# Optimization experiments

Measured on AMD Instinct MI355X. Metric: run time of the kernel, lower is better.

Reference implementation:

```python
import jax, jax.numpy as jnp
import numpy as np
import math

NUM_BINS = 10
TAIL_BOUND = 5.0
FILTER_CHANNELS = 192
KERNEL_SIZE = 3
N_LAYERS = 3
HALF = 1
MIN_BIN = 1e-3
MIN_DERIV = 1e-3


def conv1d(x, w, b, dilation=1, groups=1, padding=0):
    # x: [B,C,T], w: [O, C//groups, K]
    y = jax.lax.conv_general_dilated(
        x, w, window_strides=(1,), padding=[(padding, padding)],
        rhs_dilation=(dilation,), dimension_numbers=('NCH', 'OIH', 'NCH'),
        feature_group_count=groups)
    return y + b[None, :, None]


def ln_channels(x, g, b, eps=1e-5):
    # LayerNorm over channel dim (VITS modules.LayerNorm)
    m = jnp.mean(x, axis=1, keepdims=True)
    v = jnp.mean((x - m) ** 2, axis=1, keepdims=True)
    return g[None, :, None] * (x - m) * jax.lax.rsqrt(v + eps) + b[None, :, None]


def rq_spline(x1, uw, uh, ud):
    # piecewise rational-quadratic transform with linear tails (Durkan et al.)
    # x1: [B,1,T]; uw,uh: [B,1,T,K]; ud: [B,1,T,K-1]
    K = NUM_BINS
    tb = TAIL_BOUND
    inside = (x1 >= -tb) & (x1 <= tb)

    const = math.log(math.exp(1.0 - MIN_DERIV) - 1.0)  # softplus^-1(1-min_d)
    ud = jnp.pad(ud, [(0, 0)] * (ud.ndim - 1) + [(1, 1)], constant_values=const)

    widths = jax.nn.softmax(uw, axis=-1)
    widths = MIN_BIN + (1.0 - MIN_BIN * K) * widths
    cumw = jnp.pad(jnp.cumsum(widths, -1), [(0, 0)] * (uw.ndim - 1) + [(1, 0)])
    cumw = 2.0 * tb * cumw - tb
    cumw = cumw.at[..., 0].set(-tb).at[..., -1].set(tb)
    widths = cumw[..., 1:] - cumw[..., :-1]

    heights = jax.nn.softmax(uh, axis=-1)
    heights = MIN_BIN + (1.0 - MIN_BIN * K) * heights
    cumh = jnp.pad(jnp.cumsum(heights, -1), [(0, 0)] * (uh.ndim - 1) + [(1, 0)])
    cumh = 2.0 * tb * cumh - tb
    cumh = cumh.at[..., 0].set(-tb).at[..., -1].set(tb)
    heights = cumh[..., 1:] - cumh[..., :-1]

    derivs = MIN_DERIV + jax.nn.softplus(ud)  # [..., K+1]

    xin = jnp.clip(x1, -tb, tb)  # clamp so out-of-range lanes stay finite
    locs = cumw.at[..., -1].add(1e-6)
    bin_idx = jnp.clip(jnp.sum((xin[..., None] >= locs).astype(jnp.int32), -1) - 1, 0, K - 1)

    def take(a):
        return jnp.take_along_axis(a, bin_idx[..., None], axis=-1)[..., 0]

    icw = take(cumw)
    iw = take(widths)
    ich = take(cumh)
    ih = take(heights)
    d_l = take(derivs[..., :-1])
    d_r = take(derivs[..., 1:])
    delta = ih / iw

    theta = (xin - icw) / iw
    t1m = theta * (1.0 - theta)
    numerator = ih * (delta * theta * theta + d_l * t1m)
    denominator = delta + (d_l + d_r - 2.0 * delta) * t1m
    y = ich + numerator / denominator
    dnum = (delta * delta) * (d_r * theta * theta + 2.0 * delta * t1m + d_l * (1.0 - theta) ** 2)
    lad = jnp.log(dnum) - 2.0 * jnp.log(denominator)

    out = jnp.where(inside, y, x1)       # linear tails: identity outside
    lad = jnp.where(inside, lad, 0.0)
    return out, lad


def reference(x, x_mask, pre_w, pre_b, sep_w, sep_b, pw_w, pw_b,
              ln1_g, ln1_b, ln2_g, ln2_b, proj_w, proj_b):
    x0, x1 = x[:, :HALF], x[:, HALF:]
    h = conv1d(x0, pre_w, pre_b)
    # DDSConv (dilated depth-separable conv stack), p_dropout=0
    for i in range(N_LAYERS):
        d = KERNEL_SIZE ** i
        pad = (KERNEL_SIZE * d - d) // 2
        y = conv1d(h * x_mask, sep_w[i], sep_b[i], dilation=d,
                   groups=FILTER_CHANNELS, padding=pad)
        y = jax.nn.gelu(ln_channels(y, ln1_g[i], ln1_b[i]), approximate=False)
        y = conv1d(y, pw_w[i], pw_b[i])
        y = jax.nn.gelu(ln_channels(y, ln2_g[i], ln2_b[i]), approximate=False)
        h = h + y
    h = h * x_mask
    h = conv1d(h, proj_w, proj_b) * x_mask  # [B, half*(3K-1), T]
    b, c, t = x0.shape
    h = h.reshape(b, c, -1, t).transpose(0, 1, 3, 2)  # [B, half, T, 3K-1]
    scale = math.sqrt(FILTER_CHANNELS)
    uw = h[..., :NUM_BINS] / scale
    uh = h[..., NUM_BINS:2 * NUM_BINS] / scale
    ud = h[..., 2 * NUM_BINS:]
    x1o, lad = rq_spline(x1, uw, uh, ud)
    out = jnp.concatenate([x0, x1o], axis=1) * x_mask
    logdet = jnp.sum(lad * x_mask, axis=(1, 2))
    return out, logdet


def setup_inputs() -> dict:
    key = jax.random.key(0)
    ks = jax.random.split(key, 8)
    B, T, C, L, K = 64, 4096, FILTER_CHANNELS, N_LAYERS, KERNEL_SIZE
    return {
        'x': jax.random.normal(ks[0], (B, 2, T), jnp.float32),
        'x_mask': jnp.ones((B, 1, T), jnp.float32),
        'pre_w': jax.random.normal(ks[1], (C, 1, 1), jnp.float32) * 0.1,
        'pre_b': jnp.zeros((C,), jnp.float32),
        'sep_w': jax.random.normal(ks[2], (L, C, 1, K), jnp.float32) * 0.1,
        'sep_b': jnp.zeros((L, C), jnp.float32),
        'pw_w': jax.random.normal(ks[3], (L, C, C, 1), jnp.float32) * (1.0 / np.sqrt(C).astype(np.float32)),
        'pw_b': jnp.zeros((L, C), jnp.float32),
        'ln1_g': jnp.ones((L, C), jnp.float32),
        'ln1_b': jnp.zeros((L, C), jnp.float32),
        'ln2_g': jnp.ones((L, C), jnp.float32),
        'ln2_b': jnp.zeros((L, C), jnp.float32),
        'proj_w': jax.random.normal(ks[4], (HALF * (3 * NUM_BINS - 1), C, 1), jnp.float32) * 0.01,
        'proj_b': jnp.zeros((HALF * (3 * NUM_BINS - 1),), jnp.float32),
    }
```

## Files before the change

### kernel.cpp

```cpp
#include <hip/hip_runtime.h>
#include <stdint.h>

#define TT_ 4096
#define CC_ 192
#define TILE_ 64
#define HALO_ 13
#define TW_ 90
#define HS_ 100
#define YTS_ 200
#define NT_ 512

typedef float f32x4 __attribute__((ext_vector_type(4)));
typedef short s16x4 __attribute__((ext_vector_type(4)));
typedef short s16x8 __attribute__((ext_vector_type(8)));
typedef uint32_t ui32x2 __attribute__((ext_vector_type(2)));
typedef uint32_t ui32x4 __attribute__((ext_vector_type(4)));

__device__ __forceinline__ float bf2f(short s){
  uint32_t u = ((uint32_t)(uint16_t)s) << 16;
  float f; __builtin_memcpy(&f, &u, 4); return f;
}
__device__ __forceinline__ float bfhalf(uint32_t u, int hi){
  uint32_t v = hi ? (u & 0xFFFF0000u) : (u << 16);
  float f; __builtin_memcpy(&f, &v, 4); return f;
}
__device__ __forceinline__ short f2bf(float f){
  uint32_t u; __builtin_memcpy(&u, &f, 4);
  u += 0x7FFFu + ((u >> 16) & 1u);
  return (short)(u >> 16);
}
__device__ __forceinline__ uint32_t fbits(float f){
  uint32_t u; __builtin_memcpy(&u, &f, 4); return u;
}
__device__ __forceinline__ uint32_t pk_trunc(float lo, float hi){
  return __builtin_amdgcn_perm(fbits(hi), fbits(lo), 0x07060302u);
}
__device__ __forceinline__ uint32_t rne_u(float f){
  uint32_t u = fbits(f);
  return u + 0x7FFFu + ((u >> 16) & 1u);
}
__device__ __forceinline__ uint32_t pk_rne(float lo, float hi){
  return __builtin_amdgcn_perm(rne_u(hi), rne_u(lo), 0x07060302u);
}
__device__ __forceinline__ float gelu_f(float x){
  float t = x*x;
  float p = x*__builtin_fmaf(t, 0.0713548162f, 1.5957691216f);
  float e = __expf(-p);
  return x * __builtin_amdgcn_rcpf(1.0f + e);
}
__device__ __forceinline__ int ytix(int row, int col){
  return row*YTS_ + ((((col >> 3) ^ (row & 3)) << 3) | (col & 7));
}

template<int D>
__device__ __forceinline__ void dw_pass(const short* __restrict__ Hs, short* __restrict__ YTs,
    const float* __restrict__ sw, const float* __restrict__ sb,
    int jlo, int jhi, int tid){
  constexpr int WO = (D==9) ? 16 : 8;
  constexpr int NU = (D==9) ? 20 : 12;
  for (int g = tid; g < 96*12; g += NT_){
    int cg = g % 96, jg = g / 96;
    int j0 = jg*8;
    if (j0 + 8 <= jlo || j0 >= jhi) continue;
    int c0 = cg*2;
    uint32_t wpa[NU], wpb[NU];
    {
      const uint32_t* ra = (const uint32_t*)(Hs + (c0+0)*HS_ + j0 - WO);
      const uint32_t* rb = (const uint32_t*)(Hs + (c0+1)*HS_ + j0 - WO);
      #pragma unroll
      for (int u = 0; u < NU/2; ++u){
        ui32x2 ta = *(const ui32x2*)(ra + u*2);
        ui32x2 tb = *(const ui32x2*)(rb + u*2);
        wpa[u*2] = ta[0]; wpa[u*2+1] = ta[1];
        wpb[u*2] = tb[0]; wpb[u*2+1] = tb[1];
      }
    }
    float w0a = sw[c0*3+0], w1a = sw[c0*3+1], w2a = sw[c0*3+2], bav = sb[c0];
    float w0b = sw[c0*3+3], w1b = sw[c0*3+4], w2b = sw[c0*3+5], bbv = sb[c0+1];
    #pragma unroll
    for (int j = 0; j < 8; ++j){
      int h0 = WO + j - D, h1 = WO + j, h2 = WO + j + D;
      float va = __builtin_fmaf(w0a, bfhalf(wpa[h0>>1], h0&1),
                 __builtin_fmaf(w1a, bfhalf(wpa[h1>>1], h1&1),
                 __builtin_fmaf(w2a, bfhalf(wpa[h2>>1], h2&1), bav)));
      float vb = __builtin_fmaf(w0b, bfhalf(wpb[h0>>1], h0&1),
                 __builtin_fmaf(w1b, bfhalf(wpb[h1>>1], h1&1),
                 __builtin_fmaf(w2b, bfhalf(wpb[h2>>1], h2&1), bbv)));
      *(uint32_t*)(YTs + ytix(j0+j, c0)) = pk_trunc(va, vb);
    }
  }
}

__device__ __forceinline__ void ln_stats(const short* __restrict__ YTs, float* __restrict__ SM,
                                         float* __restrict__ SR, int jlo, int jhi, int tid){
  if (tid < 384){
    int row = tid >> 2, qtr = tid & 3;
    if (row >= jlo && row < jhi){
      float s0 = 0.f, s1 = 0.f, q0 = 0.f, q1 = 0.f;
      #pragma unroll
      for (int u=0;u<6;++u){
        s16x8 v = *(const s16x8*)(YTs + ytix(row, qtr*48 + u*8));
        #pragma unroll
        for (int e=0;e<4;e++){ float f=bf2f(v[e]); s0 += f; q0 = __builtin_fmaf(f,f,q0); }
        #pragma unroll
        for (int e=4;e<8;e++){ float f=bf2f(v[e]); s1 += f; q1 = __builtin_fmaf(f,f,q1); }
      }
      float s = s0+s1, q = q0+q1;
      s += __shfl_xor(s,1); q += __shfl_xor(q,1);
      s += __shfl_xor(s,2); q += __shfl_xor(q,2);
      if (qtr==0){
        float mean = s*(1.f/192.f);
        float var = fmaxf(q*(1.f/192.f) - mean*mean, 0.f);
        SM[row]=mean; SR[row]=rsqrtf(var+1e-5f);
      }
    }
  }
}

__global__ __launch_bounds__(512, 4)
void convflow_main(
    const float* __restrict__ x, const float* __restrict__ xmask,
    const float* __restrict__ pre_w, const float* __restrict__ pre_b,
    const float* __restrict__ sep_w, const float* __restrict__ sep_b,
    const float* __restrict__ pw_b,
    const float* __restrict__ ln1_g, const float* __restrict__ ln1_b,
    const float* __restrict__ ln2_g, const float* __restrict__ ln2_b,
    const float* __restrict__ proj_b,
    const short* __restrict__ Wbf, const short* __restrict__ Pbf,
    float* __restrict__ out, float* __restrict__ part)
{
  __shared__ __align__(16) char smem_raw[78592];
  float* MB = (float*)(smem_raw + 0);
  float* XB = (float*)(smem_raw + 640);
  float* SM = (float*)(smem_raw + 1024);
  float* SR = (float*)(smem_raw + 1408);
  short* H  = (short*)(smem_raw + 1792);
  short* YT = (short*)(smem_raw + 40192);
  float* HP = (float*)(smem_raw + 65792);

  const int tid = threadIdx.x;
  const int b = blockIdx.y, tile = blockIdx.x;
  const int t0 = tile*TILE_ - HALO_;

  for (int idx = tid; idx < 160; idx += NT_){
    int j = idx - 16; int t = t0 + j;
    float m = 0.f;
    if (j >= 0 && j < TW_ && t >= 0 && t < TT_) m = xmask[b*TT_ + t];
    MB[idx] = m;
  }
  if (tid < 96){
    int t = t0 + tid; float v = 0.f;
    if (tid < TW_ && t >= 0 && t < TT_) v = x[(b*2)*TT_ + t];
    XB[tid] = v;
  }
  __syncthreads();

  for (int g = tid; g < CC_*24; g += NT_){
    int jq = g % 24, c = g / 24;
    float w = pre_w[c], bb = pre_b[c];
    int j0 = jq*4;
    float v0 = (w*XB[j0+0] + bb)*MB[16+j0+0];
    float v1 = (w*XB[j0+1] + bb)*MB[16+j0+1];
    float v2 = (w*XB[j0+2] + bb)*MB[16+j0+2];
    float v3 = (w*XB[j0+3] + bb)*MB[16+j0+3];
    ui32x2 o; o[0] = pk_rne(v0, v1); o[1] = pk_rne(v2, v3);
    *(ui32x2*)(H + c*HS_ + j0) = o;
  }
  __syncthreads();

  #pragma unroll 1
  for (int li = 0; li < 3; ++li){
    const int jlo = (li==0) ? 1 : ((li==1) ? 4 : 13);
    const int jhi = (li==0) ? 89 : ((li==1) ? 86 : 77);
    const float* sw = sep_w + li*CC_*3;
    const float* sb = sep_b + li*CC_;

    if (li == 0)      dw_pass<1>(H, YT, sw, sb, jlo, jhi, tid);
    else if (li == 1) dw_pass<3>(H, YT, sw, sb, jlo, jhi, tid);
    else              dw_pass<9>(H, YT, sw, sb, jlo, jhi, tid);
    __syncthreads();

    ln_stats(YT, SM, SR, jlo, jhi, tid); __syncthreads();

    {
      const float* g1 = ln1_g + li*CC_;
      const float* b1 = ln1_b + li*CC_;
      for (int g = tid; g < 96*24; g += NT_){
        int ch = g % 24, row = g / 24;
        short* p = YT + ytix(row, ch*8);
        if (row >= jlo && row < jhi){
          float m = SM[row], r = SR[row];
          s16x8 v = *(s16x8*)p;
          f32x4 ga = *(const f32x4*)&g1[ch*8], gb = *(const f32x4*)&g1[ch*8+4];
          f32x4 ba = *(const f32x4*)&b1[ch*8], bb = *(const f32x4*)&b1[ch*8+4];
          float ov[8];
          #pragma unroll
          for (int e=0;e<4;e++){
            float val = (bf2f(v[e]) - m)*r*ga[e] + ba[e];
            ov[e] = gelu_f(val);
          }
          #pragma unroll
          for (int e=4;e<8;e++){
            float val = (bf2f(v[e]) - m)*r*gb[e-4] + bb[e-4];
            ov[e] = gelu_f(val);
          }
          ui32x4 o;
          #pragma unroll
          for (int e=0;e<4;e++) o[e] = pk_trunc(ov[2*e], ov[2*e+1]);
          *(ui32x4*)p = o;
        } else {
          ui32x4 z = {0u,0u,0u,0u};
          *(ui32x4*)p = z;
        }
      }
    }
    __syncthreads();

    {
      int w = tid >> 6, lane = tid & 63, l16 = lane & 15, q = lane >> 4;
      int Mh = w & 3, Nh = w >> 2;
      f32x4 acc[3][3];
      #pragma unroll
      for (int r=0;r<3;r++)
        #pragma unroll
        for (int s=0;s<3;s++){ f32x4 z = {0.f,0.f,0.f,0.f}; acc[r][s] = z; }
      const short* Wl = Wbf + li*CC_*CC_;
      #pragma unroll
      for (int kk=0;kk<6;++kk){
        s16x8 bv[3], av[3];
        #pragma unroll
        for (int s=0;s<3;++s)
          bv[s] = *(const s16x8*)&YT[ytix((Nh*3+s)*16 + l16, kk*32 + q*8)];
        #pragma unroll
        for (int r=0;r<3;++r)
          av[r] = *(const s16x8*)&Wl[((Mh*3+r)*16 + l16)*CC_ + kk*32 + q*8];
        #pragma unroll
        for (int r=0;r<3;++r)
          #pragma unroll
          for (int s=0;s<3;++s)
            acc[r][s] = __builtin_amdgcn_mfma_f32_16x16x32_bf16(av[r], bv[s], acc[r][s], 0, 0, 0);
      }
      __syncthreads();
      #pragma unroll
      for (int r=0;r<3;++r){
        int m0 = (Mh*3+r)*16 + q*4;
        f32x4 bias = *(const f32x4*)&pw_b[li*CC_ + m0];
        #pragma unroll
        for (int s=0;s<3;++s){
          int n = (Nh*3+s)*16 + l16;
          ui32x2 ov;
          ov[0] = pk_trunc(acc[r][s][0]+bias[0], acc[r][s][1]+bias[1]);
          ov[1] = pk_trunc(acc[r][s][2]+bias[2], acc[r][s][3]+bias[3]);
          *(ui32x2*)(YT + ytix(n, m0)) = ov;
        }
      }
      __syncthreads();
    }

    ln_stats(YT, SM, SR, jlo, jhi, tid); __syncthreads();

    {
      const float* g2 = ln2_g + li*CC_;
      const float* b2 = ln2_b + li*CC_;
      for (int g = tid; g < 24*48; g += NT_){
        int cgp = g % 48, jg = g / 48;
        int j0 = jg*4, c0 = cgp*4;
        if (j0 + 4 <= jlo || j0 >= jhi) continue;
        f32x4 mv = *(f32x4*)&SM[j0], rv = *(f32x4*)&SR[j0];
        f32x4 mk = *(f32x4*)&MB[16 + j0];
        f32x4 gv = *(const f32x4*)&g2[c0], bv = *(const f32x4*)&b2[c0];
        s16x4 yr[4];
        #pragma unroll
        for (int jj=0;jj<4;++jj) yr[jj] = *(s16x4*)(YT + ytix(j0+jj, c0));
        #pragma unroll
        for (int cc=0;cc<4;++cc){
          short* hp_ = H + (c0+cc)*HS_ + j0;
          s16x4 hv = *(s16x4*)hp_;
          float hf[4];
          #pragma unroll
          for (int jj=0;jj<4;++jj){
            int j = j0 + jj;
            float val = (bf2f(yr[jj][cc]) - mv[jj])*rv[jj]*gv[cc] + bv[cc];
            float hn = (bf2f(hv[jj]) + gelu_f(val))*mk[jj];
            bool ok = (j >= jlo) && (j < jhi);
            hf[jj] = ok ? hn : bf2f(hv[jj]);
          }
          ui32x2 o; o[0] = pk_rne(hf[0], hf[1]); o[1] = pk_rne(hf[2], hf[3]);
          *(ui32x2*)hp_ = o;
        }
      }
    }
    __syncthreads();
  }

  {
    int w = tid >> 6;
    if (w < 4){
      int lane = tid & 63, l16 = lane & 15, q = lane >> 4;
      int mt = w >> 1, ntp = w & 1;
      f32x4 pacc[2];
      { f32x4 z = {0.f,0.f,0.f,0.f}; pacc[0] = z; pacc[1] = z; }
      #pragma unroll
      for (int kk=0;kk<6;++kk){
        s16x8 a = *(const s16x8*)&Pbf[(mt*16 + l16)*CC_ + kk*32 + q*8];
        #pragma unroll
        for (int s=0;s<2;++s){
          int n = (ntp*2+s)*16 + l16;
          s16x8 bvv;
          #pragma unroll
          for (int i=0;i<8;++i)
            bvv[i] = H[(kk*32 + q*8 + i)*HS_ + HALO_ + n];
          pacc[s] = __builtin_amdgcn_mfma_f32_16x16x32_bf16(a, bvv, pacc[s], 0, 0, 0);
        }
      }
      #pragma unroll
      for (int s=0;s<2;++s)
        #pragma unroll
        for (int e=0;e<4;e++){
          int m = mt*16 + q*4 + e;
          if (m < 29){
            int n = (ntp*2+s)*16 + l16;
            HP[n*33 + m] = (pacc[s][e] + proj_b[m]) * MB[16 + HALO_ + n];
          }
        }
    }
  }
  __syncthreads();

  if (tid < 64){
    const int n = tid;
    const int tg = tile*TILE_ + n;
    const float msk = MB[16 + HALO_ + n];
    const float* hp = &HP[n*33];
    const float inv_s = 0.07216878364870323f;
    float uw[10], uh[10], ud9[9];
    #pragma unroll
    for (int k=0;k<10;k++){ uw[k] = hp[k]*inv_s; uh[k] = hp[10+k]*inv_s; }
    #pragma unroll
    for (int k=0;k<9;k++) ud9[k] = hp[20+k];

    float cumw[11], cumh[11];
    {
      float mx = uw[0];
      #pragma unroll
      for (int k=1;k<10;k++) mx = fmaxf(mx, uw[k]);
      float ex[10]; float ss = 0.f;
      #pragma unroll
      for (int k=0;k<10;k++){ ex[k] = __expf(uw[k]-mx); ss += ex[k]; }
      float inv = 1.0f/ss;
      cumw[0] = -5.f; float cw = 0.f;
      #pragma unroll
      for (int k=0;k<10;k++){ float wk = 0.001f + 0.99f*(ex[k]*inv); cw += wk; cumw[k+1] = 10.f*cw - 5.f; }
      cumw[10] = 5.f;
    }
    {
      float mx = uh[0];
      #pragma unroll
      for (int k=1;k<10;k++) mx = fmaxf(mx, uh[k]);
      float ex[10]; float ss = 0.f;
      #pragma unroll
      for (int k=0;k<10;k++){ ex[k] = __expf(uh[k]-mx); ss += ex[k]; }
      float inv = 1.0f/ss;
      cumh[0] = -5.f; float ch = 0.f;
      #pragma unroll
      for (int k=0;k<10;k++){ float hk = 0.001f + 0.99f*(ex[k]*inv); ch += hk; cumh[k+1] = 10.f*ch - 5.f; }
      cumh[10] = 5.f;
    }
    float dv[11];
    dv[0] = 1.0f; dv[10] = 1.0f;
    #pragma unroll
    for (int k=0;k<9;k++){
      float u = ud9[k];
      float sp = (u > 15.f) ? u : log1pf(__expf(u));
      dv[k+1] = 0.001f + sp;
    }

    const float x1 = x[(b*2+1)*TT_ + tg];
    const float xin = fminf(fmaxf(x1, -5.f), 5.f);
    int cnt = 0;
    #pragma unroll
    for (int k=0;k<11;k++){
      float lk = cumw[k] + ((k==10) ? 1e-6f : 0.f);
      cnt += (xin >= lk) ? 1 : 0;
    }
    int bin = cnt - 1;
    bin = (bin < 0) ? 0 : ((bin > 9) ? 9 : bin);

    float icw=0.f, iw=1.f, ich=0.f, ih=1.f, dl=1.f, dr=1.f;
    #pragma unroll
    for (int k=0;k<10;k++){
      if (bin == k){
        icw = cumw[k]; iw = cumw[k+1]-cumw[k];
        ich = cumh[k]; ih = cumh[k+1]-cumh[k];
        dl = dv[k]; dr = dv[k+1];
      }
    }
    float delta = ih/iw;
    float th = (xin - icw)/iw;
    float t1m = th*(1.f-th);
    float num = ih*(delta*th*th + dl*t1m);
    float den = delta + (dl + dr - 2.f*delta)*t1m;
    float yv = ich + num/den;
    float omt = 1.f - th;
    float dnum = delta*delta*(dr*th*th + 2.f*delta*t1m + dl*omt*omt);
    float lad = logf(dnum) - 2.f*logf(den);
    bool inside = (x1 >= -5.f) && (x1 <= 5.f);
    float outv = inside ? yv : x1;
    float ladv = inside ? lad : 0.f;

    out[(b*2)*TT_ + tg]   = x[(b*2)*TT_ + tg] * msk;
    out[(b*2+1)*TT_ + tg] = outv * msk;

    float lsum = ladv * msk;
    #pragma unroll
    for (int off = 32; off > 0; off >>= 1) lsum += __shfl_xor(lsum, off);
    if (tid == 0) part[b*64 + tile] = lsum;
  }
}

__global__ void convflow_pre(const float* __restrict__ pw_w, const float* __restrict__ proj_w,
                             short* __restrict__ Wbf, short* __restrict__ Pbf){
  int idx = blockIdx.x*256 + threadIdx.x;
  if (idx < 110592) Wbf[idx] = f2bf(pw_w[idx]);
  if (idx < 32*192){
    int m = idx / 192, k = idx - m*192;
    Pbf[idx] = (m < 29) ? f2bf(proj_w[m*192 + k]) : (short)0;
  }
}

__global__ void convflow_logdet(const float* __restrict__ part, float* __restrict__ out){
  int bb = threadIdx.x;
  if (bb < 64){
    float s = 0.f;
    for (int k=0;k<64;k++) s += part[bb*64 + k];
    out[524288 + bb] = s;
  }
}

extern "C" void kernel_launch(void* const* d_in, const int* in_sizes, int n_in,
                              void* d_out, int out_size, void* d_ws, size_t ws_size,
                              hipStream_t stream) {
  const float* x      = (const float*)d_in[0];
  const float* xmask  = (const float*)d_in[1];
  const float* pre_w  = (const float*)d_in[2];
  const float* pre_b  = (const float*)d_in[3];
  const float* sep_w  = (const float*)d_in[4];
  const float* sep_b  = (const float*)d_in[5];
  const float* pw_w   = (const float*)d_in[6];
  const float* pw_b   = (const float*)d_in[7];
  const float* ln1_g  = (const float*)d_in[8];
  const float* ln1_b  = (const float*)d_in[9];
  const float* ln2_g  = (const float*)d_in[10];
  const float* ln2_b  = (const float*)d_in[11];
  const float* proj_w = (const float*)d_in[12];
  const float* proj_b = (const float*)d_in[13];

  short* Wbf = (short*)d_ws;
  short* Pbf = (short*)((char*)d_ws + 221184);
  float* part = (float*)((char*)d_ws + 233472);
  float* out = (float*)d_out;

  convflow_pre<<<432, 256, 0, stream>>>(pw_w, proj_w, Wbf, Pbf);
  dim3 grid(64, 64);
  convflow_main<<<grid, NT_, 0, stream>>>(x, xmask, pre_w, pre_b, sep_w, sep_b, pw_b,
                                          ln1_g, ln1_b, ln2_g, ln2_b, proj_b,
                                          Wbf, Pbf, out, part);
  convflow_logdet<<<1, 64, 0, stream>>>(part, out);
}
```

Baseline: 595.5 us.

## Use packed fp32 math for elementwise stages and reswizzle LDS layout

Rewrites the depthwise conv, LayerNorm statistics, LN1+GELU and LN2+GELU+residual stages to work on float2 vectors with elementwise FMA, so the compiler can emit packed fp32 instructions (v_pk_fma/v_pk_mul) on CDNA. GELU now uses exp2 with a pre-scaled argument. The YT swizzle key changes from row&3 to (row^(row>>2))&3, and the LN2 loop's thread-to-tile mapping is transposed so that LDS bank conflicts are reduced. Packing and unpacking pairs may add register moves that offset the gain.

New measurement: 602.7 us. No clear change (+1.2%).

```diff
diff --git a/kernel.cpp b/kernel.cpp
--- a/kernel.cpp
+++ b/kernel.cpp
@@ -10,6 +10,7 @@
 #define YTS_ 200
 #define NT_ 512
 
+typedef float f32x2 __attribute__((ext_vector_type(2)));
 typedef float f32x4 __attribute__((ext_vector_type(4)));
 typedef short s16x4 __attribute__((ext_vector_type(4)));
 typedef short s16x8 __attribute__((ext_vector_type(8)));
@@ -42,14 +43,22 @@
 __device__ __forceinline__ uint32_t pk_rne(float lo, float hi){
   return __builtin_amdgcn_perm(rne_u(hi), rne_u(lo), 0x07060302u);
 }
-__device__ __forceinline__ float gelu_f(float x){
-  float t = x*x;
-  float p = x*__builtin_fmaf(t, 0.0713548162f, 1.5957691216f);
-  float e = __expf(-p);
-  return x * __builtin_amdgcn_rcpf(1.0f + e);
+__device__ __forceinline__ f32x2 pfma(f32x2 a, f32x2 b, f32x2 c){
+  return __builtin_elementwise_fma(a, b, c);
+}
+__device__ __forceinline__ f32x2 gelu2(f32x2 x){
+  f32x2 s = x*x;
+  f32x2 t = pfma(s, f32x2{0.0713548162f,0.0713548162f}, f32x2{1.5957691216f,1.5957691216f});
+  f32x2 p = x*t;
+  f32x2 q = p * f32x2{-1.44269504089f,-1.44269504089f};
+  f32x2 e; e[0] = __builtin_amdgcn_exp2f(q[0]); e[1] = __builtin_amdgcn_exp2f(q[1]);
+  f32x2 d = e + f32x2{1.f,1.f};
+  f32x2 r; r[0] = __builtin_amdgcn_rcpf(d[0]); r[1] = __builtin_amdgcn_rcpf(d[1]);
+  return x*r;
 }
 __device__ __forceinline__ int ytix(int row, int col){
-  return row*YTS_ + ((((col >> 3) ^ (row & 3)) << 3) | (col & 7));
+  int key = (row ^ (row >> 2)) & 3;
+  return row*YTS_ + ((((col >> 3) ^ key) << 3) | (col & 7));
 }
 
 template<int D>
@@ -75,18 +84,18 @@
         wpb[u*2] = tb[0]; wpb[u*2+1] = tb[1];
       }
     }
-    float w0a = sw[c0*3+0], w1a = sw[c0*3+1], w2a = sw[c0*3+2], bav = sb[c0];
-    float w0b = sw[c0*3+3], w1b = sw[c0*3+4], w2b = sw[c0*3+5], bbv = sb[c0+1];
+    f32x2 wv0 = { sw[c0*3+0], sw[c0*3+3] };
+    f32x2 wv1 = { sw[c0*3+1], sw[c0*3+4] };
+    f32x2 wv2 = { sw[c0*3+2], sw[c0*3+5] };
+    f32x2 bb2 = { sb[c0], sb[c0+1] };
     #pragma unroll
     for (int j = 0; j < 8; ++j){
       int h0 = WO + j - D, h1 = WO + j, h2 = WO + j + D;
-      float va = __builtin_fmaf(w0a, bfhalf(wpa[h0>>1], h0&1),
-                 __builtin_fmaf(w1a, bfhalf(wpa[h1>>1], h1&1),
-                 __builtin_fmaf(w2a, bfhalf(wpa[h2>>1], h2&1), bav)));
-      float vb = __builtin_fmaf(w0b, bfhalf(wpb[h0>>1], h0&1),
-                 __builtin_fmaf(w1b, bfhalf(wpb[h1>>1], h1&1),
-                 __builtin_fmaf(w2b, bfhalf(wpb[h2>>1], h2&1), bbv)));
-      *(uint32_t*)(YTs + ytix(j0+j, c0)) = pk_trunc(va, vb);
+      f32x2 t0 = { bfhalf(wpa[h0>>1], h0&1), bfhalf(wpb[h0>>1], h0&1) };
+      f32x2 t1 = { bfhalf(wpa[h1>>1], h1&1), bfhalf(wpb[h1>>1], h1&1) };
+      f32x2 t2 = { bfhalf(wpa[h2>>1], h2&1), bfhalf(wpb[h2>>1], h2&1) };
+      f32x2 acc = pfma(wv0, t0, pfma(wv1, t1, pfma(wv2, t2, bb2)));
+      *(uint32_t*)(YTs + ytix(j0+j, c0)) = pk_trunc(acc[0], acc[1]);
     }
   }
 }
@@ -96,16 +105,17 @@
   if (tid < 384){
     int row = tid >> 2, qtr = tid & 3;
     if (row >= jlo && row < jhi){
-      float s0 = 0.f, s1 = 0.f, q0 = 0.f, q1 = 0.f;
+      f32x2 s2 = {0.f,0.f}, q2 = {0.f,0.f};
       #pragma unroll
       for (int u=0;u<6;++u){
-        s16x8 v = *(const s16x8*)(YTs + ytix(row, qtr*48 + u*8));
-        #pragma unroll
-        for (int e=0;e<4;e++){ float f=bf2f(v[e]); s0 += f; q0 = __builtin_fmaf(f,f,q0); }
-        #pragma unroll
-        for (int e=4;e<8;e++){ float f=bf2f(v[e]); s1 += f; q1 = __builtin_fmaf(f,f,q1); }
-      }
-      float s = s0+s1, q = q0+q1;
+        ui32x4 w = *(const ui32x4*)(YTs + ytix(row, qtr*48 + u*8));
+        #pragma unroll
+        for (int k=0;k<4;++k){
+          f32x2 pr = { bfhalf(w[k],0), bfhalf(w[k],1) };
+          s2 += pr; q2 = pfma(pr, pr, q2);
+        }
+      }
+      float s = s2[0]+s2[1], q = q2[0]+q2[1];
       s += __shfl_xor(s,1); q += __shfl_xor(q,1);
       s += __shfl_xor(s,2); q += __shfl_xor(q,2);
       if (qtr==0){
@@ -190,23 +200,22 @@
         short* p = YT + ytix(row, ch*8);
         if (row >= jlo && row < jhi){
           float m = SM[row], r = SR[row];
-          s16x8 v = *(s16x8*)p;
+          f32x2 r2 = {r, r}, nm2 = {-m, -m};
           f32x4 ga = *(const f32x4*)&g1[ch*8], gb = *(const f32x4*)&g1[ch*8+4];
           f32x4 ba = *(const f32x4*)&b1[ch*8], bb = *(const f32x4*)&b1[ch*8+4];
-          float ov[8];
-          #pragma unroll
-          for (int e=0;e<4;e++){
-            float val = (bf2f(v[e]) - m)*r*ga[e] + ba[e];
-            ov[e] = gelu_f(val);
-          }
-          #pragma unroll
-          for (int e=4;e<8;e++){
-            float val = (bf2f(v[e]) - m)*r*gb[e-4] + bb[e-4];
-            ov[e] = gelu_f(val);
-          }
+          ui32x4 v = *(ui32x4*)p;
           ui32x4 o;
           #pragma unroll
-          for (int e=0;e<4;e++) o[e] = pk_trunc(ov[2*e], ov[2*e+1]);
+          for (int k=0;k<4;++k){
+            f32x2 pr = { bfhalf(v[k],0), bfhalf(v[k],1) };
+            f32x2 gk = (k<2) ? f32x2{ga[2*k], ga[2*k+1]} : f32x2{gb[2*k-4], gb[2*k-3]};
+            f32x2 bk = (k<2) ? f32x2{ba[2*k], ba[2*k+1]} : f32x2{bb[2*k-4], bb[2*k-3]};
+            f32x2 A = gk * r2;
+            f32x2 B = pfma(A, nm2, bk);
+            f32x2 val = pfma(pr, A, B);
+            f32x2 gl = gelu2(val);
+            o[k] = pk_trunc(gl[0], gl[1]);
+          }
           *(ui32x4*)p = o;
         } else {
           ui32x4 z = {0u,0u,0u,0u};
@@ -263,8 +272,8 @@
       const float* g2 = ln2_g + li*CC_;
       const float* b2 = ln2_b + li*CC_;
       for (int g = tid; g < 24*48; g += NT_){
-        int cgp = g % 48, jg = g / 48;
-        int j0 = jg*4, c0 = cgp*4;
+        int jq = g % 24, cq = g / 24;
+        int j0 = jq*4, c0 = cq*4;
         if (j0 + 4 <= jlo || j0 >= jhi) continue;
         f32x4 mv = *(f32x4*)&SM[j0], rv = *(f32x4*)&SR[j0];
         f32x4 mk = *(f32x4*)&MB[16 + j0];
@@ -272,21 +281,32 @@
         s16x4 yr[4];
         #pragma unroll
         for (int jj=0;jj<4;++jj) yr[jj] = *(s16x4*)(YT + ytix(j0+jj, c0));
+        bool ok0 = (j0   >= jlo) && (j0   < jhi);
+        bool ok1 = (j0+1 >= jlo) && (j0+1 < jhi);
+        bool ok2 = (j0+2 >= jlo) && (j0+2 < jhi);
+        bool ok3 = (j0+3 >= jlo) && (j0+3 < jhi);
         #pragma unroll
         for (int cc=0;cc<4;++cc){
           short* hp_ = H + (c0+cc)*HS_ + j0;
-          s16x4 hv = *(s16x4*)hp_;
-          float hf[4];
+          ui32x2 hw = *(ui32x2*)hp_;
+          f32x2 gcc = { gv[cc], gv[cc] }, bcc = { bv[cc], bv[cc] };
+          ui32x2 ho;
           #pragma unroll
-          for (int jj=0;jj<4;++jj){
-            int j = j0 + jj;
-            float val = (bf2f(yr[jj][cc]) - mv[jj])*rv[jj]*gv[cc] + bv[cc];
-            float hn = (bf2f(hv[jj]) + gelu_f(val))*mk[jj];
-            bool ok = (j >= jlo) && (j < jhi);
-            hf[jj] = ok ? hn : bf2f(hv[jj]);
+          for (int pp=0; pp<2; ++pp){
+            int ja = pp*2, jb = ja+1;
+            f32x2 pr = { bf2f(yr[ja][cc]), bf2f(yr[jb][cc]) };
+            f32x2 A = f32x2{rv[ja], rv[jb]} * gcc;
+            f32x2 B = pfma(A, f32x2{-mv[ja], -mv[jb]}, bcc);
+            f32x2 val = pfma(pr, A, B);
+            f32x2 gl = gelu2(val);
+            f32x2 h2 = { bfhalf(hw[pp],0), bfhalf(hw[pp],1) };
+            f32x2 hn = (h2 + gl) * f32x2{mk[ja], mk[jb]};
+            bool oa = pp ? ok2 : ok0, ob = pp ? ok3 : ok1;
+            float f0 = oa ? hn[0] : h2[0];
+            float f1 = ob ? hn[1] : h2[1];
+            ho[pp] = pk_rne(f0, f1);
           }
-          ui32x2 o; o[0] = pk_rne(hf[0], hf[1]); o[1] = pk_rne(hf[2], hf[3]);
-          *(ui32x2*)hp_ = o;
+          *(ui32x2*)hp_ = ho;
         }
       }
     }
```
